# Performance work log

Hardware: AMD Instinct MI355X
Metric: run time of the kernel (lower is better)

## Reference

```python
import jax, jax.numpy as jnp
import numpy as np

BS, DOP, RAN, AZI, ELE = 2, 32, 128, 128, 32
INTERVAL = 0.1
TAU = 1.0


def setup_inputs() -> dict:
    key = jax.random.key(0)
    ks = jax.random.split(key, 7)
    N = RAN * AZI * ELE
    seg = jax.random.normal(ks[0], (BS, N, 1), jnp.float32)
    flow = jax.random.normal(ks[1], (BS, N, 3), jnp.float32) * 2.0
    x1 = jax.random.normal(ks[2], (BS, DOP, RAN, AZI, ELE), jnp.float32)
    dop_arr = jax.random.normal(ks[3], (BS, DOP), jnp.float32)
    coords = jax.random.uniform(ks[4], (BS, 3, RAN, AZI, ELE), jnp.float32)
    ori = jax.random.normal(ks[5], (BS, 3, RAN, AZI, ELE), jnp.float32)
    u = jax.random.uniform(ks[6], (BS, DOP, RAN, AZI, ELE), jnp.float32,
                           minval=1e-6, maxval=1.0 - 1e-6)
    gumbels = -jnp.log(-jnp.log(u))  # Gumbel(0,1) noise (sampled internally in torch)
    return {"seg": seg, "flow": flow, "x1": x1, "dop_arr": dop_arr,
            "coords": coords, "ori": ori, "gumbels": gumbels}


def _gather3d(vol_flat, z, y, x, H, W):
    # vol_flat: (B, C, D*H*W); z,y,x: (B, D, H, W) int32
    B = vol_flat.shape[0]
    idx = ((z * H + y) * W + x).reshape(B, 1, -1)
    g = jnp.take_along_axis(vol_flat, idx, axis=2)
    return g  # (B, C, N)


def _grid_sample_3d_border(vol, gx, gy, gz):
    # Trilinear grid_sample, padding_mode='border', align_corners=True.
    # vol: (B, C, D, H, W); gx/gy/gz: (B, D, H, W) normalized coords in [-1, 1]
    B, C, D, H, W = vol.shape
    ix = jnp.clip((gx + 1.0) * 0.5 * (W - 1), 0.0, W - 1.0)
    iy = jnp.clip((gy + 1.0) * 0.5 * (H - 1), 0.0, H - 1.0)
    iz = jnp.clip((gz + 1.0) * 0.5 * (D - 1), 0.0, D - 1.0)
    x0f, y0f, z0f = jnp.floor(ix), jnp.floor(iy), jnp.floor(iz)
    wx, wy, wz = ix - x0f, iy - y0f, iz - z0f
    x0 = jnp.clip(x0f.astype(jnp.int32), 0, W - 1)
    y0 = jnp.clip(y0f.astype(jnp.int32), 0, H - 1)
    z0 = jnp.clip(z0f.astype(jnp.int32), 0, D - 1)
    x1 = jnp.clip(x0 + 1, 0, W - 1)
    y1 = jnp.clip(y0 + 1, 0, H - 1)
    z1 = jnp.clip(z0 + 1, 0, D - 1)
    vf = vol.reshape(B, C, -1)
    out = jnp.zeros((B, C, D * H * W), vol.dtype)
    for zc, wzc in ((z0, 1.0 - wz), (z1, wz)):
        for yc, wyc in ((y0, 1.0 - wy), (y1, wy)):
            for xc, wxc in ((x0, 1.0 - wx), (x1, wx)):
                w = (wzc * wyc * wxc).reshape(B, 1, -1)
                out = out + w * _gather3d(vf, zc, yc, xc, H, W)
    return out.reshape(B, C, D, H, W)


def _warp_flowxyz(coords, flo):
    B, C, D, H, W = coords.shape
    zz = jnp.arange(D, dtype=jnp.float32)[:, None, None]
    yy = jnp.arange(H, dtype=jnp.float32)[None, :, None]
    xx = jnp.arange(W, dtype=jnp.float32)[None, None, :]
    # vgrid = base grid + flow, per channel (x, y, z)
    vx = xx + flo[:, 0]
    vy = yy + flo[:, 1]
    vz = zz + flo[:, 2]
    gx = 2.0 * vx / (W - 1) - 1.0
    gy = 2.0 * vy / (H - 1) - 1.0
    gz = 2.0 * vz / (D - 1) - 1.0
    r, a, e = coords[:, 0], coords[:, 1], coords[:, 2]
    ce = jnp.cos(e)
    xyz = jnp.stack([r * ce * jnp.cos(a), r * ce * jnp.sin(a), r * jnp.sin(e)], axis=1)
    xyz_new = _grid_sample_3d_border(xyz, gx, gy, gz)
    return xyz_new - xyz


def reference(seg, flow, x1, dop_arr, coords, ori, gumbels):
    bs, dop, ran, azi, ele = x1.shape
    dop_b = dop_arr.reshape(bs, dop, 1, 1, 1)
    # gumbel_softmax(hard=True): forward value is the hard one-hot
    y_soft = jax.nn.softmax((x1 + gumbels) / TAU, axis=1)
    idx = jnp.argmax(y_soft, axis=1)
    y_hard = jax.nn.one_hot(idx, dop, axis=1, dtype=x1.dtype)
    max_x1 = y_hard + y_soft - jax.lax.stop_gradient(y_soft)  # straight-through
    softmax_x1 = jax.nn.softmax(x1, axis=1)
    x1_dop1 = jnp.sum(max_x1 * dop_b, axis=1, keepdims=True)
    x1_dop2 = jnp.sum(softmax_x1 * dop_b, axis=1, keepdims=True)
    x1_dop = jnp.concatenate([x1_dop1, x1_dop2], axis=1)  # (bs, 2, R, A, E)
    seg_v = jnp.transpose(seg, (0, 2, 1)).reshape(bs, -1, ran, azi, ele)
    flow_v = jnp.transpose(flow, (0, 2, 1)).reshape(bs, -1, ran, azi, ele)
    flow_xyz = _warp_flowxyz(coords, flow_v)
    velo = flow_xyz / INTERVAL
    dop_label = jnp.sum(velo * ori, axis=1, keepdims=True)
    dop_error = (dop_label - x1_dop) ** 2
    seg_label = jax.nn.sigmoid(10.0 * (0.15 - dop_error))
    seg_label = jnp.mean(seg_label, axis=1, keepdims=True)
    seg_sig = jax.nn.sigmoid(seg_v)
    loss = jnp.mean(jnp.abs(seg_sig - seg_label))
    return loss
```

## Files before the change

kernel.cpp:

```cpp
#include <hip/hip_runtime.h>
#include <math.h>

#define BSZ  2
#define DOPN 32
#define RAN  128
#define AZI  128
#define ELE  32
#define NVOX (RAN * AZI * ELE)
#define TPB  256
#define VPT  4
#define DH   8

__device__ __forceinline__ float sigmoidf_(float t) {
    return 1.0f / (1.0f + __expf(-t));
}

__global__ __launch_bounds__(TPB) void xyz_precompute(
    const float* __restrict__ coords, float4* __restrict__ xyz4)
{
    const int n0 = (blockIdx.x * TPB + threadIdx.x) * 4;
    const int b = blockIdx.y;
    const float* cb = coords + (size_t)b * 3 * NVOX;
    const float4 r4 = *(const float4*)(cb + n0);
    const float4 a4 = *(const float4*)(cb + NVOX + n0);
    const float4 e4 = *(const float4*)(cb + 2 * NVOX + n0);
    const float rr[4] = { r4.x, r4.y, r4.z, r4.w };
    const float aa[4] = { a4.x, a4.y, a4.z, a4.w };
    const float ee[4] = { e4.x, e4.y, e4.z, e4.w };
    float4* op = xyz4 + (size_t)b * NVOX + n0;
    #pragma unroll
    for (int v = 0; v < 4; ++v) {
        float sa, ca, se, ce;
        __sincosf(aa[v], &sa, &ca);
        __sincosf(ee[v], &se, &ce);
        op[v] = make_float4(rr[v] * ce * ca, rr[v] * ce * sa, rr[v] * se, 0.0f);
    }
}

__global__ __launch_bounds__(TPB) void seg_dop_loss(
    const float* __restrict__ seg, const float* __restrict__ flow,
    const float* __restrict__ x1, const float* __restrict__ dop_arr,
    const float* __restrict__ ori, const float* __restrict__ gumbels,
    const float4* __restrict__ xyz4, float* __restrict__ out)
{
    __shared__ float s_dop[DOPN];
    __shared__ float s_wave[TPB / 64];

    const int b = blockIdx.y;
    if (threadIdx.x < DOPN) s_dop[threadIdx.x] = dop_arr[b * DOPN + threadIdx.x];
    __syncthreads();

    const int n0 = (blockIdx.x * TPB + threadIdx.x) * VPT;
    const size_t base = (size_t)b * DOPN * NVOX + (size_t)n0;

    float m_lg[VPT] = { -3.4e38f, -3.4e38f, -3.4e38f, -3.4e38f };
    float mdop[VPT] = { 0.f, 0.f, 0.f, 0.f };
    float ssum[VPT] = { 0.f, 0.f, 0.f, 0.f };
    float wsum[VPT] = { 0.f, 0.f, 0.f, 0.f };

    for (int h = 0; h < DOPN / DH; ++h) {
        const size_t dbase = base + (size_t)h * DH * NVOX;
        float4 xa[DH], ga[DH];
        #pragma unroll
        for (int d = 0; d < DH; ++d)
            xa[d] = *(const float4*)(x1 + dbase + (size_t)d * NVOX);
        #pragma unroll
        for (int d = 0; d < DH; ++d)
            ga[d] = *(const float4*)(gumbels + dbase + (size_t)d * NVOX);
        #pragma unroll
        for (int d = 0; d < DH; ++d) {
            const float dv = s_dop[h * DH + d];
            const float xv[VPT] = { xa[d].x, xa[d].y, xa[d].z, xa[d].w };
            const float gv[VPT] = { ga[d].x, ga[d].y, ga[d].z, ga[d].w };
            #pragma unroll
            for (int v = 0; v < VPT; ++v) {
                const float lg = xv[v] + gv[v];
                if (lg > m_lg[v]) { m_lg[v] = lg; mdop[v] = dv; }
                const float ev = __expf(xv[v]);
                ssum[v] += ev;
                wsum[v] += ev * dv;
            }
        }
    }

    const float* fl = flow + ((size_t)b * NVOX + (size_t)n0) * 3;
    float fbuf[3 * VPT];
    *(float4*)(fbuf + 0) = *(const float4*)(fl + 0);
    *(float4*)(fbuf + 4) = *(const float4*)(fl + 4);
    *(float4*)(fbuf + 8) = *(const float4*)(fl + 8);

    const float4* xb4 = xyz4 + (size_t)b * NVOX;
    float4 bxyz[VPT];
    #pragma unroll
    for (int v = 0; v < VPT; ++v) bxyz[v] = xb4[n0 + v];

    const float* ob = ori + (size_t)b * 3 * NVOX;
    const float4 oX4 = *(const float4*)(ob + n0);
    const float4 oY4 = *(const float4*)(ob + NVOX + n0);
    const float4 oZ4 = *(const float4*)(ob + 2 * NVOX + n0);
    const float oX[VPT] = { oX4.x, oX4.y, oX4.z, oX4.w };
    const float oY[VPT] = { oY4.x, oY4.y, oY4.z, oY4.w };
    const float oZ[VPT] = { oZ4.x, oZ4.y, oZ4.z, oZ4.w };

    const float4 sg4 = *(const float4*)(seg + (size_t)b * NVOX + n0);
    const float sg[VPT] = { sg4.x, sg4.y, sg4.z, sg4.w };

    const int xB = n0 & (ELE - 1);
    const int yI = (n0 >> 5) & (AZI - 1);
    const int zI = n0 >> 12;

    float contrib = 0.0f;
    #pragma unroll
    for (int v = 0; v < VPT; ++v) {
        const float vx = (float)(xB + v) + fbuf[3 * v + 0];
        const float vy = (float)yI       + fbuf[3 * v + 1];
        const float vz = (float)zI       + fbuf[3 * v + 2];

        const float gx = 2.0f * vx / (float)(ELE - 1) - 1.0f;
        const float gy = 2.0f * vy / (float)(AZI - 1) - 1.0f;
        const float gz = 2.0f * vz / (float)(RAN - 1) - 1.0f;
        const float ix = fminf(fmaxf((gx + 1.0f) * 0.5f * (float)(ELE - 1), 0.0f), (float)(ELE - 1));
        const float iy = fminf(fmaxf((gy + 1.0f) * 0.5f * (float)(AZI - 1), 0.0f), (float)(AZI - 1));
        const float iz = fminf(fmaxf((gz + 1.0f) * 0.5f * (float)(RAN - 1), 0.0f), (float)(RAN - 1));

        const float x0f = floorf(ix), y0f = floorf(iy), z0f = floorf(iz);
        const float wx = ix - x0f, wy = iy - y0f, wz = iz - z0f;
        int x0 = (int)x0f; x0 = x0 < 0 ? 0 : (x0 > ELE - 1 ? ELE - 1 : x0);
        int y0 = (int)y0f; y0 = y0 < 0 ? 0 : (y0 > AZI - 1 ? AZI - 1 : y0);
        int z0 = (int)z0f; z0 = z0 < 0 ? 0 : (z0 > RAN - 1 ? RAN - 1 : z0);
        const int x1c = x0 + 1 > ELE - 1 ? ELE - 1 : x0 + 1;
        const int y1c = y0 + 1 > AZI - 1 ? AZI - 1 : y0 + 1;
        const int z1c = z0 + 1 > RAN - 1 ? RAN - 1 : z0 + 1;

        const int m00 = (z0  * AZI + y0 ) * ELE;
        const int m01 = (z0  * AZI + y1c) * ELE;
        const int m10 = (z1c * AZI + y0 ) * ELE;
        const int m11 = (z1c * AZI + y1c) * ELE;
        const float4 c000 = xb4[m00 + x0],  c001 = xb4[m00 + x1c];
        const float4 c010 = xb4[m01 + x0],  c011 = xb4[m01 + x1c];
        const float4 c100 = xb4[m10 + x0],  c101 = xb4[m10 + x1c];
        const float4 c110 = xb4[m11 + x0],  c111 = xb4[m11 + x1c];

        const float w000 = (1.0f - wz) * (1.0f - wy) * (1.0f - wx);
        const float w001 = (1.0f - wz) * (1.0f - wy) * wx;
        const float w010 = (1.0f - wz) * wy * (1.0f - wx);
        const float w011 = (1.0f - wz) * wy * wx;
        const float w100 = wz * (1.0f - wy) * (1.0f - wx);
        const float w101 = wz * (1.0f - wy) * wx;
        const float w110 = wz * wy * (1.0f - wx);
        const float w111 = wz * wy * wx;

        const float sX = w000*c000.x + w001*c001.x + w010*c010.x + w011*c011.x
                       + w100*c100.x + w101*c101.x + w110*c110.x + w111*c111.x;
        const float sY = w000*c000.y + w001*c001.y + w010*c010.y + w011*c011.y
                       + w100*c100.y + w101*c101.y + w110*c110.y + w111*c111.y;
        const float sZ = w000*c000.z + w001*c001.z + w010*c010.z + w011*c011.z
                       + w100*c100.z + w101*c101.z + w110*c110.z + w111*c111.z;

        const float vX = (sX - bxyz[v].x) * 10.0f;
        const float vY = (sY - bxyz[v].y) * 10.0f;
        const float vZ = (sZ - bxyz[v].z) * 10.0f;
        const float dop_label = vX * oX[v] + vY * oY[v] + vZ * oZ[v];

        const float dop1 = mdop[v];
        const float dop2 = wsum[v] / ssum[v];
        float e1 = dop_label - dop1; e1 *= e1;
        float e2 = dop_label - dop2; e2 *= e2;
        const float seg_label = 0.5f * (sigmoidf_(10.0f * (0.15f - e1)) +
                                        sigmoidf_(10.0f * (0.15f - e2)));
        contrib += fabsf(sigmoidf_(sg[v]) - seg_label);
    }

    #pragma unroll
    for (int off = 32; off > 0; off >>= 1)
        contrib += __shfl_down(contrib, off, 64);
    const int lane = threadIdx.x & 63;
    const int wid  = threadIdx.x >> 6;
    if (lane == 0) s_wave[wid] = contrib;
    __syncthreads();
    if (threadIdx.x == 0) {
        float bsum = 0.0f;
        #pragma unroll
        for (int w = 0; w < TPB / 64; ++w) bsum += s_wave[w];
        atomicAdd(out, bsum * (1.0f / ((float)BSZ * (float)NVOX)));
    }
}

extern "C" void kernel_launch(void* const* d_in, const int* in_sizes, int n_in,
                              void* d_out, int out_size, void* d_ws, size_t ws_size,
                              hipStream_t stream) {
    const float* seg    = (const float*)d_in[0];
    const float* flow   = (const float*)d_in[1];
    const float* x1     = (const float*)d_in[2];
    const float* dopar  = (const float*)d_in[3];
    const float* coords = (const float*)d_in[4];
    const float* ori    = (const float*)d_in[5];
    const float* gumb   = (const float*)d_in[6];
    float* out = (float*)d_out;
    float4* xyz4 = (float4*)d_ws;

    hipMemsetAsync(d_out, 0, sizeof(float) * (size_t)out_size, stream);

    dim3 gridA(NVOX / (TPB * 4), BSZ);
    xyz_precompute<<<gridA, TPB, 0, stream>>>(coords, xyz4);
    dim3 gridB(NVOX / (TPB * VPT), BSZ);
    seg_dop_loss<<<gridB, TPB, 0, stream>>>(seg, flow, x1, dopar, ori, gumb, xyz4, out);
}
```

Baseline: 343.9 us.

## Halve voxels per thread, split x1/gumbel loads across lane pairs, fold memset

Each thread now handles 2 voxels instead of 4, which doubles the block count. Paired lanes share the work of loading x1 and gumbels: one lane loads the x1 float4 and the other loads the gumbel float4 for the same 4 voxels, and they swap halves with __shfl_xor. This keeps each load a full float4 while halving the number of loads per thread and its register footprint. The separate hipMemsetAsync is removed; block 0 of the precompute kernel now zeroes the output, saving a launch. In exchange the inner loop gains extra shuffles and selects.

```diff
diff --git a/kernel.cpp b/kernel.cpp
--- a/kernel.cpp
+++ b/kernel.cpp
@@ -8,7 +8,7 @@
 #define ELE  32
 #define NVOX (RAN * AZI * ELE)
 #define TPB  256
-#define VPT  4
+#define VPT  2
 #define DH   8
 
 __device__ __forceinline__ float sigmoidf_(float t) {
@@ -16,8 +16,12 @@
 }
 
 __global__ __launch_bounds__(TPB) void xyz_precompute(
-    const float* __restrict__ coords, float4* __restrict__ xyz4)
+    const float* __restrict__ coords, float4* __restrict__ xyz4,
+    float* __restrict__ out, int out_elems)
 {
+    if (blockIdx.x == 0 && blockIdx.y == 0) {
+        for (int i = threadIdx.x; i < out_elems; i += TPB) out[i] = 0.0f;
+    }
     const int n0 = (blockIdx.x * TPB + threadIdx.x) * 4;
     const int b = blockIdx.y;
     const float* cb = coords + (size_t)b * 3 * NVOX;
@@ -51,27 +55,31 @@
     __syncthreads();
 
     const int n0 = (blockIdx.x * TPB + threadIdx.x) * VPT;
-    const size_t base = (size_t)b * DOPN * NVOX + (size_t)n0;
-
-    float m_lg[VPT] = { -3.4e38f, -3.4e38f, -3.4e38f, -3.4e38f };
-    float mdop[VPT] = { 0.f, 0.f, 0.f, 0.f };
-    float ssum[VPT] = { 0.f, 0.f, 0.f, 0.f };
-    float wsum[VPT] = { 0.f, 0.f, 0.f, 0.f };
-
+
+    float m_lg[VPT] = { -3.4e38f, -3.4e38f };
+    float mdop[VPT] = { 0.f, 0.f };
+    float ssum[VPT] = { 0.f, 0.f };
+    float wsum[VPT] = { 0.f, 0.f };
+
+    const int par = threadIdx.x & 1;
+    const int cg  = n0 & ~3;
+    const float* swp = par ? gumbels : x1;
+    const size_t sbase = (size_t)b * DOPN * NVOX + (size_t)cg;
+
+    float4 q[DH];
     for (int h = 0; h < DOPN / DH; ++h) {
-        const size_t dbase = base + (size_t)h * DH * NVOX;
-        float4 xa[DH], ga[DH];
         #pragma unroll
         for (int d = 0; d < DH; ++d)
-            xa[d] = *(const float4*)(x1 + dbase + (size_t)d * NVOX);
-        #pragma unroll
-        for (int d = 0; d < DH; ++d)
-            ga[d] = *(const float4*)(gumbels + dbase + (size_t)d * NVOX);
+            q[d] = *(const float4*)(swp + sbase + (size_t)(h * DH + d) * NVOX);
         #pragma unroll
         for (int d = 0; d < DH; ++d) {
             const float dv = s_dop[h * DH + d];
-            const float xv[VPT] = { xa[d].x, xa[d].y, xa[d].z, xa[d].w };
-            const float gv[VPT] = { ga[d].x, ga[d].y, ga[d].z, ga[d].w };
+            const float t0 = par ? q[d].x : q[d].z;
+            const float t1 = par ? q[d].y : q[d].w;
+            const float r0 = __shfl_xor(t0, 1, 64);
+            const float r1 = __shfl_xor(t1, 1, 64);
+            const float xv[VPT] = { par ? r0 : q[d].x, par ? r1 : q[d].y };
+            const float gv[VPT] = { par ? q[d].z : r0, par ? q[d].w : r1 };
             #pragma unroll
             for (int v = 0; v < VPT; ++v) {
                 const float lg = xv[v] + gv[v];
@@ -85,9 +93,9 @@
 
     const float* fl = flow + ((size_t)b * NVOX + (size_t)n0) * 3;
     float fbuf[3 * VPT];
-    *(float4*)(fbuf + 0) = *(const float4*)(fl + 0);
-    *(float4*)(fbuf + 4) = *(const float4*)(fl + 4);
-    *(float4*)(fbuf + 8) = *(const float4*)(fl + 8);
+    *(float2*)(fbuf)     = *(const float2*)(fl);
+    *(float2*)(fbuf + 2) = *(const float2*)(fl + 2);
+    *(float2*)(fbuf + 4) = *(const float2*)(fl + 4);
 
     const float4* xb4 = xyz4 + (size_t)b * NVOX;
     float4 bxyz[VPT];
@@ -95,15 +103,15 @@
     for (int v = 0; v < VPT; ++v) bxyz[v] = xb4[n0 + v];
 
     const float* ob = ori + (size_t)b * 3 * NVOX;
-    const float4 oX4 = *(const float4*)(ob + n0);
-    const float4 oY4 = *(const float4*)(ob + NVOX + n0);
-    const float4 oZ4 = *(const float4*)(ob + 2 * NVOX + n0);
-    const float oX[VPT] = { oX4.x, oX4.y, oX4.z, oX4.w };
-    const float oY[VPT] = { oY4.x, oY4.y, oY4.z, oY4.w };
-    const float oZ[VPT] = { oZ4.x, oZ4.y, oZ4.z, oZ4.w };
-
-    const float4 sg4 = *(const float4*)(seg + (size_t)b * NVOX + n0);
-    const float sg[VPT] = { sg4.x, sg4.y, sg4.z, sg4.w };
+    const float2 oX2 = *(const float2*)(ob + n0);
+    const float2 oY2 = *(const float2*)(ob + NVOX + n0);
+    const float2 oZ2 = *(const float2*)(ob + 2 * NVOX + n0);
+    const float oX[VPT] = { oX2.x, oX2.y };
+    const float oY[VPT] = { oY2.x, oY2.y };
+    const float oZ[VPT] = { oZ2.x, oZ2.y };
+
+    const float2 sg2 = *(const float2*)(seg + (size_t)b * NVOX + n0);
+    const float sg[VPT] = { sg2.x, sg2.y };
 
     const int xB = n0 & (ELE - 1);
     const int yI = (n0 >> 5) & (AZI - 1);
@@ -199,10 +207,8 @@
     float* out = (float*)d_out;
     float4* xyz4 = (float4*)d_ws;
 
-    hipMemsetAsync(d_out, 0, sizeof(float) * (size_t)out_size, stream);
-
     dim3 gridA(NVOX / (TPB * 4), BSZ);
-    xyz_precompute<<<gridA, TPB, 0, stream>>>(coords, xyz4);
+    xyz_precompute<<<gridA, TPB, 0, stream>>>(coords, xyz4, out, out_size);
     dim3 gridB(NVOX / (TPB * VPT), BSZ);
     seg_dop_loss<<<gridB, TPB, 0, stream>>>(seg, flow, x1, dopar, ori, gumb, xyz4, out);
 }
```

After: 324.5 us. 1.06x faster.
